# Kernel tuning notes

Measured on AMD Instinct MI355X. Metric: run time of the kernel, lower is better.

## Reference

```python
import jax, jax.numpy as jnp
import numpy as np

D_IN = 512
SEQ_LEN = 4096
CHUNK = 256
NUM_CHUNKS = SEQ_LEN // CHUNK
BATCH = 4


def _xavier_uniform(key, d_in, d_out):
    limit = float(np.sqrt(6.0 / (d_in + d_out)))
    return jax.random.uniform(key, (d_in, d_out), dtype=jnp.float32, minval=-limit, maxval=limit)


def _logit(p, eps=1e-06):
    p = min(max(p, eps), 1.0 - eps)
    return jnp.asarray(np.log(p / (1.0 - p)), dtype=jnp.float32)


def setup_inputs() -> dict:
    key = jax.random.key(0)
    ks = jax.random.split(key, 6)
    x = jax.random.normal(ks[0], (BATCH, SEQ_LEN, D_IN), dtype=jnp.float32)
    return {
        "x": x,
        "w_q": _xavier_uniform(ks[1], D_IN, D_IN),
        "w_k": _xavier_uniform(ks[2], D_IN, D_IN),
        "w_v": _xavier_uniform(ks[3], D_IN, D_IN),
        "mem_w1": _xavier_uniform(ks[4], D_IN, 2 * D_IN),
        "mem_w2": _xavier_uniform(ks[5], 2 * D_IN, D_IN),
        "alpha_t": _logit(0.001),  # unconstrained; sigmoid -> alpha
        "lr_t": _logit(0.01),
        "decay_t": _logit(0.9),
        "update_mem": 1,
    }


def _mem_fwd(h, W1, W2):
    # LinearMLPMemory depth=2: x @ W1 -> gelu -> @ W2 (torch F.gelu is exact erf)
    return jax.nn.gelu(h @ W1, approximate=False) @ W2


def reference(x, w_q, w_k, w_v, mem_w1, mem_w2, alpha_t, lr_t, decay_t, update_mem):
    alpha = jax.nn.sigmoid(alpha_t)
    lr = jax.nn.sigmoid(lr_t)
    decay = jax.nn.sigmoid(decay_t)

    def loss_fn(Ws, k, v):
        W1, W2 = Ws
        pred = _mem_fwd(k, W1, W2)
        return jnp.mean((pred - v) ** 2)

    grad_fn = jax.grad(loss_fn)

    def step(carry, chunk):
        # chunk: [B, CHUNK, D]
        W1, W2, S1, S2 = carry
        k = chunk @ w_k
        v = chunk @ w_v
        g1, g2 = grad_fn((W1, W2), k, v)
        S1 = decay * S1 - lr * g1  # surprise (momentum of negative grads)
        S2 = decay * S2 - lr * g2
        W1 = (1.0 - alpha) * W1 + S1  # weight decay + surprise update
        W2 = (1.0 - alpha) * W2 + S2
        return (W1, W2, S1, S2), None

    W1, W2 = mem_w1, mem_w2
    if update_mem:
        B, S, D = x.shape
        # [NUM_CHUNKS, B, CHUNK, D]: sequential store over chunks (parallelize=False)
        chunks = x.reshape(B, NUM_CHUNKS, CHUNK, D).transpose(1, 0, 2, 3)
        init = (W1, W2, jnp.zeros_like(W1), jnp.zeros_like(W2))
        (W1, W2, _, _), _ = jax.lax.scan(step, init, chunks)

    q = x @ w_q
    return _mem_fwd(q, W1, W2)
```

## Files before the change

kernel.cpp:

```cpp
#include <hip/hip_runtime.h>
#include <math.h>

#define D_IN    512
#define HID     1024
#define CHUNK_L 256
#define NCHUNK  16
#define SEQ_L   4096
#define ROWS    1024
#define NROWS_T 16384

typedef __attribute__((ext_vector_type(4))) float f32x4;
typedef __attribute__((ext_vector_type(8))) short bf16x8;
typedef __attribute__((ext_vector_type(4))) short bf16x4;

#define LOSS_SCALE (2.0f / 524288.0f)

__device__ __forceinline__ float gelu_f(float v) {
    return v * 0.5f * (1.0f + erff(v * 0.70710678118654752f));
}
__device__ __forceinline__ float dgelu_f(float v) {
    float cdf = 0.5f * (1.0f + erff(v * 0.70710678118654752f));
    float pdf = 0.3989422804014327f * expf(-0.5f * v * v);
    return cdf + v * pdf;
}
__device__ __forceinline__ float sigmoid_dev(float x) { return 1.0f / (1.0f + expf(-x)); }
__device__ __forceinline__ short f2b(float f) {
    unsigned u = __float_as_uint(f);
    u += 0x7fffu + ((u >> 16) & 1u);
    return (short)(u >> 16);
}
__device__ __forceinline__ float b2f(short s) {
    return __uint_as_float(((unsigned)(unsigned short)s) << 16);
}
__device__ __forceinline__ float read_scalar(const float* p) {
    float v = *p;
    if (fabsf(v) > 0.5f && fabsf(v) < 16.0f) return v;
    unsigned short lo = ((const unsigned short*)p)[0];
    return __uint_as_float(((unsigned)lo) << 16);
}

__device__ __forceinline__ void glds16(const short* g, short* l) {
    __builtin_amdgcn_global_load_lds(
        (const __attribute__((address_space(1))) void*)g,
        (__attribute__((address_space(3))) void*)l, 16, 0, 0);
}

#define VMWAIT(N) asm volatile("s_waitcnt vmcnt(" #N ")" ::: "memory")

template<int NKB, int NSLOT>
__device__ __forceinline__ void tile_gemm2(
    const short* __restrict__ A, int lda,
    const short* __restrict__ B, int ldb,
    int m0, int n0, short* KB, f32x4 acc[2][2])
{
    const int tid = threadIdx.x;
    const int lane = tid & 63, wave = tid >> 6;
    const int wy = (wave >> 1) * 32, wx = (wave & 1) * 32;
    const int l16 = lane & 15, q = lane >> 4;

    const int ga = tid, gb = tid + 256;
    const int ra = ga >> 3, ja = ga & 7;
    const int rb = gb >> 3, jb = gb & 7;
    const short* sA0 = A + (size_t)(m0 + ra) * lda + ((ja ^ (ra & 7)) << 3);
    const short* sA1 = A + (size_t)(m0 + rb) * lda + ((jb ^ (rb & 7)) << 3);
    const short* sB0 = B + (size_t)(n0 + ra) * ldb + ((ja ^ (ra & 7)) << 3);
    const short* sB1 = B + (size_t)(n0 + rb) * ldb + ((jb ^ (rb & 7)) << 3);

    f32x4 z = {0.f, 0.f, 0.f, 0.f};
    acc[0][0] = z; acc[0][1] = z; acc[1][0] = z; acc[1][1] = z;

    auto issue = [&](int kb) {
        const int ko = kb << 6;
        short* d = KB + (kb % NSLOT) * 8192 + wave * 512;
        glds16(sA0 + ko, d);
        glds16(sA1 + ko, d + 2048);
        glds16(sB0 + ko, d + 4096);
        glds16(sB1 + ko, d + 6144);
    };
#pragma unroll
    for (int kb = 0; kb < NSLOT - 1 && kb < NKB; ++kb) issue(kb);

#pragma unroll
    for (int j = 0; j < NKB; ++j) {
        int ah = NKB - 1 - j; if (ah > NSLOT - 2) ah = NSLOT - 2;
        if      (ah >= 6) VMWAIT(24);
        else if (ah == 5) VMWAIT(20);
        else if (ah == 4) VMWAIT(16);
        else if (ah == 3) VMWAIT(12);
        else if (ah == 2) VMWAIT(8);
        else if (ah == 1) VMWAIT(4);
        else              VMWAIT(0);
        __builtin_amdgcn_s_barrier();
        __builtin_amdgcn_sched_barrier(0);
        if (j + NSLOT - 1 < NKB) issue(j + NSLOT - 1);
        const short* sl = KB + (j % NSLOT) * 8192;
#pragma unroll
        for (int ks = 0; ks < 2; ++ks) {
            bf16x8 af[2], bf[2];
#pragma unroll
            for (int i = 0; i < 2; ++i) {
                int row = wy + i * 16 + l16;
                af[i] = *(const bf16x8*)&sl[(row << 6) + (((ks * 4 + q) ^ (row & 7)) << 3)];
            }
#pragma unroll
            for (int jj = 0; jj < 2; ++jj) {
                int row = wx + jj * 16 + l16;
                bf[jj] = *(const bf16x8*)&sl[4096 + (row << 6) + (((ks * 4 + q) ^ (row & 7)) << 3)];
            }
#pragma unroll
            for (int i = 0; i < 2; ++i)
#pragma unroll
                for (int jj = 0; jj < 2; ++jj)
                    acc[i][jj] = __builtin_amdgcn_mfma_f32_16x16x32_bf16(af[i], bf[jj], acc[i][jj], 0, 0, 0);
        }
    }
}

#define EPI_IDX() \
    const int tid_ = threadIdx.x; \
    const int wy_  = ((tid_ >> 6) >> 1) * 32; \
    const int wxl_ = ((tid_ >> 6) & 1) * 32; \
    const int q4_  = ((tid_ & 63) >> 4) * 4; \
    const int l16_ = tid_ & 15;

__global__ __launch_bounds__(256)
void init_all(const float* __restrict__ w_q, const float* __restrict__ w_k,
              const float* __restrict__ w_v, const float* __restrict__ m1,
              const float* __restrict__ m2,
              float* __restrict__ W1f, float* __restrict__ W2f,
              float* __restrict__ S1, float* __restrict__ S2,
              short* __restrict__ WkvT, short* __restrict__ wqT,
              short* __restrict__ W1bT, short* __restrict__ W2bT,
              short* __restrict__ W2b0, short* __restrict__ W2b1)
{
    int i = blockIdx.x * 256 + threadIdx.x;
    float w1 = m1[i], w2 = m2[i];
    W1f[i] = w1; S1[i] = 0.f;
    W2f[i] = w2; S2[i] = 0.f;
    short w2b = f2b(w2);
    W2b0[i] = w2b; W2b1[i] = w2b;
    int n9 = i >> 9, k9 = i & 511;
    W1bT[i] = f2b(m1[(size_t)k9 * HID + n9]);
    WkvT[i] = f2b(n9 < 512 ? w_k[(size_t)k9 * D_IN + n9]
                           : w_v[(size_t)k9 * D_IN + (n9 - 512)]);
    if (i < 262144) wqT[i] = f2b(w_q[(size_t)k9 * D_IN + n9]);
    int n10 = i >> 10, k10 = i & 1023;
    W2bT[i] = f2b(m2[(size_t)k10 * D_IN + n10]);
}

__global__ __launch_bounds__(256)
void xb_kernel(const float* __restrict__ x, short* __restrict__ xb)
{
    int i = blockIdx.x * 256 + threadIdx.x;
    f32x4 a = ((const f32x4*)x)[i * 2];
    f32x4 b = ((const f32x4*)x)[i * 2 + 1];
    bf16x8 o;
#pragma unroll
    for (int u = 0; u < 4; ++u) { o[u] = f2b(a[u]); o[u + 4] = f2b(b[u]); }
    ((bf16x8*)xb)[i] = o;
}

__global__ __launch_bounds__(256)
void kvq_kernel(const short* __restrict__ xb, const short* __restrict__ WkvT,
                const short* __restrict__ wqT,
                short* __restrict__ KVall, short* __restrict__ Ktall,
                short* __restrict__ qall)
{
    __shared__ short KB[3 * 8192];
    const int bid = blockIdx.x;
    EPI_IDX();
    f32x4 acc[2][2];
    if (bid < 4096) {
        int t = bid >> 8, tile = bid & 255;
        int m0 = (tile & 15) * 64, n0 = (tile >> 4) * 64;
        const short* Akv = xb + ((size_t)(m0 >> 8) * SEQ_L + (size_t)t * CHUNK_L + (m0 & 255)) * D_IN;
        tile_gemm2<8, 3>(Akv, D_IN, WkvT, D_IN, 0, n0, KB, acc);
        short* KV = KVall + (size_t)t * ROWS * 1024;
        short* Kt = Ktall + (size_t)t * D_IN * 1024;
#pragma unroll
        for (int i = 0; i < 2; ++i)
#pragma unroll
            for (int j = 0; j < 2; ++j) {
                int m = m0 + wy_ + i * 16 + q4_, n = n0 + wxl_ + j * 16 + l16_;
                bf16x4 pk;
#pragma unroll
                for (int r = 0; r < 4; ++r) {
                    short b = f2b(acc[i][j][r]);
                    KV[(size_t)(m + r) * 1024 + n] = b;
                    pk[r] = b;
                }
                if (n < 512) *(bf16x4*)&Kt[(size_t)n * 1024 + m] = pk;
            }
    } else {
        int idx = bid - 4096;
        int m0 = (idx & 255) * 64, n0 = (idx >> 8) * 64;
        tile_gemm2<8, 3>(xb, D_IN, wqT, D_IN, m0, n0, KB, acc);
#pragma unroll
        for (int i = 0; i < 2; ++i)
#pragma unroll
            for (int j = 0; j < 2; ++j) {
                int m = m0 + wy_ + i * 16 + q4_, n = n0 + wxl_ + j * 16 + l16_;
#pragma unroll
                for (int r = 0; r < 4; ++r)
                    qall[(size_t)(m + r) * D_IN + n] = f2b(acc[i][j][r]);
            }
    }
}

__global__ __launch_bounds__(256)
void h_kernel(const short* __restrict__ KVt, const short* __restrict__ W1bT,
              short* __restrict__ Gb, short* __restrict__ GbT, short* __restrict__ DG)
{
    __shared__ short KB[8 * 8192];
    const int bid = blockIdx.x;
    EPI_IDX();
    int m0 = (bid & 15) * 64, n0 = (bid >> 4) * 64;
    f32x4 acc[2][2];
    tile_gemm2<8, 8>(KVt, 1024, W1bT, D_IN, m0, n0, KB, acc);
#pragma unroll
    for (int i = 0; i < 2; ++i)
#pragma unroll
        for (int j = 0; j < 2; ++j) {
            int m = m0 + wy_ + i * 16 + q4_, n = n0 + wxl_ + j * 16 + l16_;
            bf16x4 pg;
#pragma unroll
            for (int r = 0; r < 4; ++r) {
                float v = acc[i][j][r];
                float g = gelu_f(v);
                Gb[(size_t)(m + r) * 1024 + n] = f2b(g);
                DG[(size_t)(m + r) * 1024 + n] = f2b(dgelu_f(v));
                pg[r] = f2b(g);
            }
            *(bf16x4*)&GbT[(size_t)n * 1024 + m] = pg;
        }
}

__global__ __launch_bounds__(256)
void e_kernel(const short* __restrict__ Gb, const short* __restrict__ W2bT,
              short* __restrict__ KVt, short* __restrict__ EVt)
{
    __shared__ short KB[8 * 8192];
    const int bid = blockIdx.x;
    EPI_IDX();
    int m0 = (bid & 15) * 64, n0 = (bid >> 4) * 64;
    f32x4 acc[2][2];
    tile_gemm2<16, 8>(Gb, HID, W2bT, HID, m0, n0, KB, acc);
#pragma unroll
    for (int i = 0; i < 2; ++i)
#pragma unroll
        for (int j = 0; j < 2; ++j) {
            int m = m0 + wy_ + i * 16 + q4_, n = n0 + wxl_ + j * 16 + l16_;
            bf16x4 pe;
#pragma unroll
            for (int r = 0; r < 4; ++r) {
                size_t ci = (size_t)(m + r) * 1024 + 512 + n;
                float e = (acc[i][j][r] - b2f(KVt[ci])) * LOSS_SCALE;
                KVt[ci] = f2b(e);
                pe[r] = f2b(e);
            }
            *(bf16x4*)&EVt[(size_t)n * 1024 + m] = pe;
        }
}

__global__ __launch_bounds__(256)
void dhg2_kernel(const short* __restrict__ KVt, const short* __restrict__ W2bP,
                 const short* __restrict__ DG, short* __restrict__ DHt,
                 const short* __restrict__ GbT, const short* __restrict__ EVt,
                 float* __restrict__ W2f, float* __restrict__ S2,
                 short* __restrict__ W2bT, short* __restrict__ W2bN,
                 const float* __restrict__ ap, const float* __restrict__ lp,
                 const float* __restrict__ dp, const int* __restrict__ um)
{
    __shared__ short KB[4 * 8192];
    const int bid = blockIdx.x;
    EPI_IDX();
    f32x4 acc[2][2];
    if (bid < 256) {
        int m0 = (bid & 15) * 64, n0 = (bid >> 4) * 64;
        tile_gemm2<8, 4>(KVt + 512, 1024, W2bP, D_IN, m0, n0, KB, acc);
#pragma unroll
        for (int i = 0; i < 2; ++i)
#pragma unroll
            for (int j = 0; j < 2; ++j) {
                int m = m0 + wy_ + i * 16 + q4_, n = n0 + wxl_ + j * 16 + l16_;
                bf16x4 pd;
#pragma unroll
                for (int r = 0; r < 4; ++r)
                    pd[r] = f2b(acc[i][j][r] * b2f(DG[(size_t)(m + r) * 1024 + n]));
                *(bf16x4*)&DHt[(size_t)n * 1024 + m] = pd;
            }
    } else {
        int idx = bid - 256;
        int m0 = (idx & 15) * 64, n0 = (idx >> 4) * 64;
        tile_gemm2<16, 4>(GbT, ROWS, EVt, ROWS, m0, n0, KB, acc);
        if (*um != 0) {
            const float alpha = sigmoid_dev(read_scalar(ap));
            const float lr    = sigmoid_dev(read_scalar(lp));
            const float decay = sigmoid_dev(read_scalar(dp));
#pragma unroll
            for (int i = 0; i < 2; ++i)
#pragma unroll
                for (int j = 0; j < 2; ++j) {
                    int m = m0 + wy_ + i * 16 + q4_, n = n0 + wxl_ + j * 16 + l16_;
                    bf16x4 pw;
#pragma unroll
                    for (int r = 0; r < 4; ++r) {
                        size_t ci = (size_t)(m + r) * D_IN + n;
                        float s = decay * S2[ci] - lr * acc[i][j][r];
                        S2[ci] = s;
                        float w = (1.0f - alpha) * W2f[ci] + s;
                        W2f[ci] = w;
                        W2bN[ci] = f2b(w);
                        pw[r] = f2b(w);
                    }
                    *(bf16x4*)&W2bT[(size_t)n * 1024 + m] = pw;
                }
        }
    }
}

__global__ __launch_bounds__(256)
void g1_kernel(const short* __restrict__ Ktt, const short* __restrict__ DHt,
               float* __restrict__ W1f, float* __restrict__ S1,
               short* __restrict__ W1bT,
               const float* __restrict__ ap, const float* __restrict__ lp,
               const float* __restrict__ dp, const int* __restrict__ um)
{
    __shared__ short KB[8 * 8192];
    const int bid = blockIdx.x;
    EPI_IDX();
    int m0 = (bid & 7) * 64, n0 = (bid >> 3) * 64;
    f32x4 acc[2][2];
    tile_gemm2<16, 8>(Ktt, ROWS, DHt, ROWS, m0, n0, KB, acc);
    if (*um != 0) {
        const float alpha = sigmoid_dev(read_scalar(ap));
        const float lr    = sigmoid_dev(read_scalar(lp));
        const float decay = sigmoid_dev(read_scalar(dp));
#pragma unroll
        for (int i = 0; i < 2; ++i)
#pragma unroll
            for (int j = 0; j < 2; ++j) {
                int m = m0 + wy_ + i * 16 + q4_, n = n0 + wxl_ + j * 16 + l16_;
                bf16x4 pw;
#pragma unroll
                for (int r = 0; r < 4; ++r) {
                    size_t ci = (size_t)(m + r) * HID + n;
                    float s = decay * S1[ci] - lr * acc[i][j][r];
                    S1[ci] = s;
                    float w = (1.0f - alpha) * W1f[ci] + s;
                    W1f[ci] = w;
                    pw[r] = f2b(w);
                }
                *(bf16x4*)&W1bT[(size_t)n * D_IN + m] = pw;
            }
    }
}

__global__ __launch_bounds__(256)
void ro_h_kernel(const short* __restrict__ qall, const short* __restrict__ W1bT,
                 short* __restrict__ Hro)
{
    __shared__ short KB[3 * 8192];
    const int bid = blockIdx.x;
    EPI_IDX();
    int m0 = (bid & 255) * 64, n0 = (bid >> 8) * 64;
    f32x4 acc[2][2];
    tile_gemm2<8, 3>(qall, D_IN, W1bT, D_IN, m0, n0, KB, acc);
#pragma unroll
    for (int i = 0; i < 2; ++i)
#pragma unroll
        for (int j = 0; j < 2; ++j) {
            int m = m0 + wy_ + i * 16 + q4_, n = n0 + wxl_ + j * 16 + l16_;
#pragma unroll
            for (int r = 0; r < 4; ++r)
                Hro[(size_t)(m + r) * HID + n] = f2b(gelu_f(acc[i][j][r]));
        }
}

__global__ __launch_bounds__(256)
void ro_o_kernel(const short* __restrict__ Hro, const short* __restrict__ W2bT,
                 float* __restrict__ out)
{
    __shared__ short KB[3 * 8192];
    const int bid = blockIdx.x;
    EPI_IDX();
    int m0 = (bid & 255) * 64, n0 = (bid >> 8) * 64;
    f32x4 acc[2][2];
    tile_gemm2<16, 3>(Hro, HID, W2bT, HID, m0, n0, KB, acc);
#pragma unroll
    for (int i = 0; i < 2; ++i)
#pragma unroll
        for (int j = 0; j < 2; ++j) {
            int m = m0 + wy_ + i * 16 + q4_, n = n0 + wxl_ + j * 16 + l16_;
#pragma unroll
            for (int r = 0; r < 4; ++r)
                out[(size_t)(m + r) * D_IN + n] = acc[i][j][r];
        }
}

extern "C" void kernel_launch(void* const* d_in, const int* in_sizes, int n_in,
                              void* d_out, int out_size, void* d_ws, size_t ws_size,
                              hipStream_t stream)
{
    const float* x      = (const float*)d_in[0];
    const float* w_q    = (const float*)d_in[1];
    const float* w_k    = (const float*)d_in[2];
    const float* w_v    = (const float*)d_in[3];
    const float* mem_w1 = (const float*)d_in[4];
    const float* mem_w2 = (const float*)d_in[5];
    const float* ap     = (const float*)d_in[6];
    const float* lp     = (const float*)d_in[7];
    const float* dpp    = (const float*)d_in[8];
    const int*   um     = (const int*)d_in[9];
    float* out = (float*)d_out;

    const int nW = D_IN * HID;
    float* W1f = (float*)d_ws;
    float* W2f = W1f + nW;
    float* S1  = W2f + nW;
    float* S2  = S1 + nW;
    short* p   = (short*)(S2 + nW);
    short* WkvT = p;            p += nW;
    short* wqT  = p;            p += 256 * 1024;
    short* W1bT = p;            p += nW;
    short* W2bT = p;            p += nW;
    short* W2b0 = p;            p += nW;
    short* W2b1 = p;            p += nW;
    short* Gb   = p;            p += ROWS * HID;
    short* GbT  = p;            p += ROWS * HID;
    short* DG   = p;            p += ROWS * HID;
    short* EVt  = p;            p += ROWS * D_IN;
    short* DHt  = p;            p += ROWS * HID;
    short* qall = p;            p += (size_t)NROWS_T * D_IN;
    short* KVall = p;           p += (size_t)NCHUNK * ROWS * 1024;
    short* Ktall = p;           p += (size_t)NCHUNK * D_IN * 1024;
    short* Hro  = p;            p += (size_t)NROWS_T * HID;
    short* xb   = p;            p += (size_t)NROWS_T * D_IN;

    dim3 blk(256);
    hipLaunchKernelGGL(init_all, dim3(nW / 256), blk, 0, stream,
                       w_q, w_k, w_v, mem_w1, mem_w2,
                       W1f, W2f, S1, S2, WkvT, wqT, W1bT, W2bT, W2b0, W2b1);
    hipLaunchKernelGGL(xb_kernel, dim3(4096), blk, 0, stream, x, xb);
    hipLaunchKernelGGL(kvq_kernel, dim3(6144), blk, 0, stream,
                       xb, WkvT, wqT, KVall, Ktall, qall);

    for (int t = 0; t < NCHUNK; ++t) {
        short* KVt  = KVall + (size_t)t * ROWS * 1024;
        short* Ktt  = Ktall + (size_t)t * D_IN * 1024;
        short* W2bP = (t & 1) ? W2b1 : W2b0;
        short* W2bN = (t & 1) ? W2b0 : W2b1;
        hipLaunchKernelGGL(h_kernel, dim3(256), blk, 0, stream, KVt, W1bT, Gb, GbT, DG);
        hipLaunchKernelGGL(e_kernel, dim3(128), blk, 0, stream, Gb, W2bT, KVt, EVt);
        hipLaunchKernelGGL(dhg2_kernel, dim3(384), blk, 0, stream,
                           KVt, W2bP, DG, DHt, GbT, EVt, W2f, S2, W2bT, W2bN,
                           ap, lp, dpp, um);
        hipLaunchKernelGGL(g1_kernel, dim3(128), blk, 0, stream,
                           Ktt, DHt, W1f, S1, W1bT, ap, lp, dpp, um);
    }

    hipLaunchKernelGGL(ro_h_kernel, dim3(4096), blk, 0, stream, qall, W1bT, Hro);
    hipLaunchKernelGGL(ro_o_kernel, dim3(2048), blk, 0, stream, Hro, W2bT, out);
}
```

Before: 795.3 us.

## Regroup per-chunk kernels: separate dH, fuse W2 and W1 gradient updates

The per-chunk kernel sequence is regrouped. The dH GEMM becomes its own kernel, and the W2 gradient/update GEMM runs alongside the W1 gradient/update GEMM in one 256-block launch. Because W2 is no longer read and written in the same launch, the ping-pong bf16 copies of W2 collapse into a single buffer. Pipeline depth also rises from 4 to 8 stages for the dH and g2 GEMMs. The aim is to balance block counts per launch and cut per-chunk launch imbalance, at the cost of larger shared-memory use, which may lower occupancy.

Measured after the change: 749.4 us. 5.8% less time.

```diff
diff --git a/kernel.cpp b/kernel.cpp
--- a/kernel.cpp
+++ b/kernel.cpp
@@ -131,14 +131,13 @@
               float* __restrict__ S1, float* __restrict__ S2,
               short* __restrict__ WkvT, short* __restrict__ wqT,
               short* __restrict__ W1bT, short* __restrict__ W2bT,
-              short* __restrict__ W2b0, short* __restrict__ W2b1)
+              short* __restrict__ W2bn)
 {
     int i = blockIdx.x * 256 + threadIdx.x;
     float w1 = m1[i], w2 = m2[i];
     W1f[i] = w1; S1[i] = 0.f;
     W2f[i] = w2; S2[i] = 0.f;
-    short w2b = f2b(w2);
-    W2b0[i] = w2b; W2b1[i] = w2b;
+    W2bn[i] = f2b(w2);
     int n9 = i >> 9, k9 = i & 511;
     W1bT[i] = f2b(m1[(size_t)k9 * HID + n9]);
     WkvT[i] = f2b(n9 < 512 ? w_k[(size_t)k9 * D_IN + n9]
@@ -263,36 +262,45 @@
 }
 
 __global__ __launch_bounds__(256)
-void dhg2_kernel(const short* __restrict__ KVt, const short* __restrict__ W2bP,
-                 const short* __restrict__ DG, short* __restrict__ DHt,
-                 const short* __restrict__ GbT, const short* __restrict__ EVt,
-                 float* __restrict__ W2f, float* __restrict__ S2,
-                 short* __restrict__ W2bT, short* __restrict__ W2bN,
-                 const float* __restrict__ ap, const float* __restrict__ lp,
-                 const float* __restrict__ dp, const int* __restrict__ um)
-{
-    __shared__ short KB[4 * 8192];
-    const int bid = blockIdx.x;
-    EPI_IDX();
-    f32x4 acc[2][2];
-    if (bid < 256) {
+void dh_kernel(const short* __restrict__ KVt, const short* __restrict__ W2bn,
+               const short* __restrict__ DG, short* __restrict__ DHt)
+{
+    __shared__ short KB[8 * 8192];
+    const int bid = blockIdx.x;
+    EPI_IDX();
+    int m0 = (bid & 15) * 64, n0 = (bid >> 4) * 64;
+    f32x4 acc[2][2];
+    tile_gemm2<8, 8>(KVt + 512, 1024, W2bn, D_IN, m0, n0, KB, acc);
+#pragma unroll
+    for (int i = 0; i < 2; ++i)
+#pragma unroll
+        for (int j = 0; j < 2; ++j) {
+            int m = m0 + wy_ + i * 16 + q4_, n = n0 + wxl_ + j * 16 + l16_;
+            bf16x4 pd;
+#pragma unroll
+            for (int r = 0; r < 4; ++r)
+                pd[r] = f2b(acc[i][j][r] * b2f(DG[(size_t)(m + r) * 1024 + n]));
+            *(bf16x4*)&DHt[(size_t)n * 1024 + m] = pd;
+        }
+}
+
+__global__ __launch_bounds__(256)
+void g21_kernel(const short* __restrict__ GbT, const short* __restrict__ EVt,
+                const short* __restrict__ Ktt, const short* __restrict__ DHt,
+                float* __restrict__ W2f, float* __restrict__ S2,
+                short* __restrict__ W2bT, short* __restrict__ W2bn,
+                float* __restrict__ W1f, float* __restrict__ S1,
+                short* __restrict__ W1bT,
+                const float* __restrict__ ap, const float* __restrict__ lp,
+                const float* __restrict__ dp, const int* __restrict__ um)
+{
+    __shared__ short KB[8 * 8192];
+    const int bid = blockIdx.x;
+    EPI_IDX();
+    f32x4 acc[2][2];
+    if (bid < 128) {
         int m0 = (bid & 15) * 64, n0 = (bid >> 4) * 64;
-        tile_gemm2<8, 4>(KVt + 512, 1024, W2bP, D_IN, m0, n0, KB, acc);
-#pragma unroll
-        for (int i = 0; i < 2; ++i)
-#pragma unroll
-            for (int j = 0; j < 2; ++j) {
-                int m = m0 + wy_ + i * 16 + q4_, n = n0 + wxl_ + j * 16 + l16_;
-                bf16x4 pd;
-#pragma unroll
-                for (int r = 0; r < 4; ++r)
-                    pd[r] = f2b(acc[i][j][r] * b2f(DG[(size_t)(m + r) * 1024 + n]));
-                *(bf16x4*)&DHt[(size_t)n * 1024 + m] = pd;
-            }
-    } else {
-        int idx = bid - 256;
-        int m0 = (idx & 15) * 64, n0 = (idx >> 4) * 64;
-        tile_gemm2<16, 4>(GbT, ROWS, EVt, ROWS, m0, n0, KB, acc);
+        tile_gemm2<16, 8>(GbT, ROWS, EVt, ROWS, m0, n0, KB, acc);
         if (*um != 0) {
             const float alpha = sigmoid_dev(read_scalar(ap));
             const float lr    = sigmoid_dev(read_scalar(lp));
@@ -310,49 +318,38 @@
                         S2[ci] = s;
                         float w = (1.0f - alpha) * W2f[ci] + s;
                         W2f[ci] = w;
-                        W2bN[ci] = f2b(w);
+                        W2bn[ci] = f2b(w);
                         pw[r] = f2b(w);
                     }
                     *(bf16x4*)&W2bT[(size_t)n * 1024 + m] = pw;
                 }
         }
-    }
-}
-
-__global__ __launch_bounds__(256)
-void g1_kernel(const short* __restrict__ Ktt, const short* __restrict__ DHt,
-               float* __restrict__ W1f, float* __restrict__ S1,
-               short* __restrict__ W1bT,
-               const float* __restrict__ ap, const float* __restrict__ lp,
-               const float* __restrict__ dp, const int* __restrict__ um)
-{
-    __shared__ short KB[8 * 8192];
-    const int bid = blockIdx.x;
-    EPI_IDX();
-    int m0 = (bid & 7) * 64, n0 = (bid >> 3) * 64;
-    f32x4 acc[2][2];
-    tile_gemm2<16, 8>(Ktt, ROWS, DHt, ROWS, m0, n0, KB, acc);
-    if (*um != 0) {
-        const float alpha = sigmoid_dev(read_scalar(ap));
-        const float lr    = sigmoid_dev(read_scalar(lp));
-        const float decay = sigmoid_dev(read_scalar(dp));
-#pragma unroll
-        for (int i = 0; i < 2; ++i)
-#pragma unroll
-            for (int j = 0; j < 2; ++j) {
-                int m = m0 + wy_ + i * 16 + q4_, n = n0 + wxl_ + j * 16 + l16_;
-                bf16x4 pw;
-#pragma unroll
-                for (int r = 0; r < 4; ++r) {
-                    size_t ci = (size_t)(m + r) * HID + n;
-                    float s = decay * S1[ci] - lr * acc[i][j][r];
-                    S1[ci] = s;
-                    float w = (1.0f - alpha) * W1f[ci] + s;
-                    W1f[ci] = w;
-                    pw[r] = f2b(w);
+    } else {
+        int idx = bid - 128;
+        int m0 = (idx & 7) * 64, n0 = (idx >> 3) * 64;
+        tile_gemm2<16, 8>(Ktt, ROWS, DHt, ROWS, m0, n0, KB, acc);
+        if (*um != 0) {
+            const float alpha = sigmoid_dev(read_scalar(ap));
+            const float lr    = sigmoid_dev(read_scalar(lp));
+            const float decay = sigmoid_dev(read_scalar(dp));
+#pragma unroll
+            for (int i = 0; i < 2; ++i)
+#pragma unroll
+                for (int j = 0; j < 2; ++j) {
+                    int m = m0 + wy_ + i * 16 + q4_, n = n0 + wxl_ + j * 16 + l16_;
+                    bf16x4 pw;
+#pragma unroll
+                    for (int r = 0; r < 4; ++r) {
+                        size_t ci = (size_t)(m + r) * HID + n;
+                        float s = decay * S1[ci] - lr * acc[i][j][r];
+                        S1[ci] = s;
+                        float w = (1.0f - alpha) * W1f[ci] + s;
+                        W1f[ci] = w;
+                        pw[r] = f2b(w);
+                    }
+                    *(bf16x4*)&W1bT[(size_t)n * D_IN + m] = pw;
                 }
-                *(bf16x4*)&W1bT[(size_t)n * D_IN + m] = pw;
-            }
+        }
     }
 }
 
@@ -424,8 +421,7 @@
     short* wqT  = p;            p += 256 * 1024;
     short* W1bT = p;            p += nW;
     short* W2bT = p;            p += nW;
-    short* W2b0 = p;            p += nW;
-    short* W2b1 = p;            p += nW;
+    short* W2bn = p;            p += nW;
     short* Gb   = p;            p += ROWS * HID;
     short* GbT  = p;            p += ROWS * HID;
     short* DG   = p;            p += ROWS * HID;
@@ -440,7 +436,7 @@
     dim3 blk(256);
     hipLaunchKernelGGL(init_all, dim3(nW / 256), blk, 0, stream,
                        w_q, w_k, w_v, mem_w1, mem_w2,
-                       W1f, W2f, S1, S2, WkvT, wqT, W1bT, W2bT, W2b0, W2b1);
+                       W1f, W2f, S1, S2, WkvT, wqT, W1bT, W2bT, W2bn);
     hipLaunchKernelGGL(xb_kernel, dim3(4096), blk, 0, stream, x, xb);
     hipLaunchKernelGGL(kvq_kernel, dim3(6144), blk, 0, stream,
                        xb, WkvT, wqT, KVall, Ktall, qall);
@@ -448,15 +444,12 @@
     for (int t = 0; t < NCHUNK; ++t) {
         short* KVt  = KVall + (size_t)t * ROWS * 1024;
         short* Ktt  = Ktall + (size_t)t * D_IN * 1024;
-        short* W2bP = (t & 1) ? W2b1 : W2b0;
-        short* W2bN = (t & 1) ? W2b0 : W2b1;
         hipLaunchKernelGGL(h_kernel, dim3(256), blk, 0, stream, KVt, W1bT, Gb, GbT, DG);
         hipLaunchKernelGGL(e_kernel, dim3(128), blk, 0, stream, Gb, W2bT, KVt, EVt);
-        hipLaunchKernelGGL(dhg2_kernel, dim3(384), blk, 0, stream,
-                           KVt, W2bP, DG, DHt, GbT, EVt, W2f, S2, W2bT, W2bN,
-                           ap, lp, dpp, um);
-        hipLaunchKernelGGL(g1_kernel, dim3(128), blk, 0, stream,
-                           Ktt, DHt, W1f, S1, W1bT, ap, lp, dpp, um);
+        hipLaunchKernelGGL(dh_kernel, dim3(256), blk, 0, stream, KVt, W2bn, DG, DHt);
+        hipLaunchKernelGGL(g21_kernel, dim3(256), blk, 0, stream,
+                           GbT, EVt, Ktt, DHt, W2f, S2, W2bT, W2bn,
+                           W1f, S1, W1bT, ap, lp, dpp, um);
     }
 
     hipLaunchKernelGGL(ro_h_kernel, dim3(4096), blk, 0, stream, qall, W1bT, Hro);
```
